# Performance work log

Hardware: AMD Instinct MI355X
Metric: run time of the kernel (lower is better)

Reference implementation:

```python
import jax, jax.numpy as jnp
import numpy as np

B, T, D = 256, 500, 3   # batch, time steps, input features (time, mag, err)
U, C = 512, 10          # PhasedLSTM units, n_classes
R_ON = 0.05             # open ratio of the phased time gate
ALPHA = 1e-3            # leak rate during closed phase
LN_EPS = 1e-3           # keras LayerNormalization default epsilon


def _glorot(key, shape):
    lim = np.sqrt(6.0 / (shape[0] + shape[1])).astype(np.float32)
    return jax.random.uniform(key, shape, jnp.float32, -lim, lim)


def setup_inputs() -> dict:
    key = jax.random.key(0)
    ks = jax.random.split(key, 12)
    x = jax.random.normal(ks[0], (B, T, D), jnp.float32)
    # monotonically increasing observation times per sample
    times = jnp.cumsum(jax.random.uniform(ks[1], (B, T), jnp.float32), axis=1)
    # layer 0 PhasedLSTM params (gate order i, f, g, o)
    W0 = _glorot(ks[2], (D, 4 * U)); R0 = _glorot(ks[3], (U, 4 * U)); b0 = jnp.zeros((4 * U,), jnp.float32)
    tau0 = jnp.exp(jax.random.uniform(ks[4], (U,), jnp.float32, 0.0, 3.0))
    s0 = jax.random.uniform(ks[5], (U,), jnp.float32) * tau0
    # layer 1
    W1 = _glorot(ks[6], (U, 4 * U)); R1 = _glorot(ks[7], (U, 4 * U)); b1 = jnp.zeros((4 * U,), jnp.float32)
    tau1 = jnp.exp(jax.random.uniform(ks[8], (U,), jnp.float32, 0.0, 3.0))
    s1 = jax.random.uniform(ks[9], (U,), jnp.float32) * tau1
    # per-layer LayerNorm params
    g0 = jnp.ones((U,), jnp.float32); be0 = jnp.zeros((U,), jnp.float32)
    g1 = jnp.ones((U,), jnp.float32); be1 = jnp.zeros((U,), jnp.float32)
    # classifier head
    Wf = _glorot(ks[10], (U, C)); bf = jnp.zeros((C,), jnp.float32)
    return dict(x=x, times=times, W0=W0, R0=R0, b0=b0, tau0=tau0, s0=s0, g0=g0, be0=be0,
                W1=W1, R1=R1, b1=b1, tau1=tau1, s1=s1, g1=g1, be1=be1, Wf=Wf, bf=bf)


def _layernorm(h, g, b):
    m = jnp.mean(h, axis=-1, keepdims=True)
    v = jnp.var(h, axis=-1, keepdims=True)
    return (h - m) * jax.lax.rsqrt(v + LN_EPS) * g + b


def _time_gate(t, tau, s):
    # t: [B], tau/s: [U] -> k: [B, U]
    phi = jnp.mod(t[:, None] - s, tau) / tau
    return jnp.where(phi < 0.5 * R_ON, 2.0 * phi / R_ON,
                     jnp.where(phi < R_ON, 2.0 - 2.0 * phi / R_ON, ALPHA * phi))


def _plstm_step(xi, ti, h, c, W, R, b, tau, s):
    z = xi @ W + h @ R + b                       # [B, 4U]
    i, f, g, o = jnp.split(z, 4, axis=-1)
    i = jax.nn.sigmoid(i); f = jax.nn.sigmoid(f); o = jax.nn.sigmoid(o)
    c_new = f * c + i * jnp.tanh(g)
    h_new = o * jnp.tanh(c_new)
    k = _time_gate(ti, tau, s)                   # phased time gate
    return k * h_new + (1.0 - k) * h, k * c_new + (1.0 - k) * c


def reference(x, times, W0, R0, b0, tau0, s0, g0, be0,
              W1, R1, b1, tau1, s1, g1, be1, Wf, bf):
    xt = jnp.transpose(x, (1, 0, 2))  # [T, B, D]
    tt = times.T                      # [T, B]
    zeros = jnp.zeros((x.shape[0], U), x.dtype)
    init = (zeros, zeros, zeros, zeros)

    def step(carry, inp):
        h0, c0, h1, c1 = carry
        xi, ti = inp
        h0n, c0n = _plstm_step(xi, ti, h0, c0, W0, R0, b0, tau0, s0)
        a0 = _layernorm(h0n, g0, be0)   # normed output feeds next layer; raw state is carried
        h1n, c1n = _plstm_step(a0, ti, h1, c1, W1, R1, b1, tau1, s1)
        a1 = _layernorm(h1n, g1, be1)
        probs = jax.nn.softmax(a1 @ Wf + bf)  # dropout is identity at inference
        return (h0n, c0n, h1n, c1n), probs

    _, out = jax.lax.scan(step, init, (xt, tt))  # out: [T, B, C]
    return jnp.transpose(out, (1, 0, 2))
```

## Files before the change

### kernel.cpp

```cpp
#include <hip/hip_runtime.h>
#include <hip/hip_bf16.h>


#define NB 256
#define NTHR 384
#define T_STEPS 500
#define RON 0.05f
#define ALPHA_LEAK 1e-3f

typedef short short8 __attribute__((ext_vector_type(8)));
typedef float f32x4 __attribute__((ext_vector_type(4)));
typedef unsigned long long ull;

#define OFF_WSWZ 0u
#define OFF_U1   6291456u
#define OFF_V1   6299648u
#define OFF_WFP  6307840u
#define OFF_UFV  6328320u
#define OFF_H0B  6328448u
#define OFF_H1B  6852736u
#define OFF_ST0  7377024u
#define OFF_ST1  7508096u
#define OFF_FLG0 7639168u
#define OFF_FLG1 7640192u
#define ZERO_BYTES 1312768u

#define SMEM_BYTES 156160

#define AT_LD(p)    __hip_atomic_load((p), __ATOMIC_RELAXED, __HIP_MEMORY_SCOPE_AGENT)
#define AT_ST(p, v) __hip_atomic_store((p), (v), __ATOMIC_RELAXED, __HIP_MEMORY_SCOPE_AGENT)

#define G2L(gp, lp) \
  __builtin_amdgcn_global_load_lds( \
      (const __attribute__((address_space(1))) void*)(gp), \
      (__attribute__((address_space(3))) void*)(lp), 16, 0, 16)

__device__ __forceinline__ short f2bf(float x) {
  unsigned u = __float_as_uint(x);
  unsigned r = (u + 0x7fffu + ((u >> 16) & 1u)) >> 16;
  return (short)r;
}
__device__ __forceinline__ float bf2f(short s) {
  return __uint_as_float(((unsigned)(unsigned short)s) << 16);
}
__device__ __forceinline__ float sigm(float x) { return 1.f / (1.f + __expf(-x)); }
__device__ __forceinline__ float tanh_f(float x) {
  float cx = fminf(fmaxf(x, -15.f), 15.f);
  float e = __expf(2.f * cx);
  return (e - 1.f) / (e + 1.f);
}
__device__ __forceinline__ float timegate(float t, float tau, float s) {
  float phi = fmodf(t - s, tau);
  if (phi < 0.f) phi += tau;
  phi /= tau;
  return phi < 0.5f * RON ? (2.f / RON) * phi
       : (phi < RON ? 2.f - (2.f / RON) * phi : ALPHA_LEAK * phi);
}
__device__ __forceinline__ int fragidx(int m, int k) {
  return ((((k >> 5) * 2 + (m >> 4)) * 64) + (((k >> 3) & 3) * 16) + (m & 15)) * 8 + (k & 7);
}

__global__ void prep_weights(const float* __restrict__ R0, const float* __restrict__ W1,
                             const float* __restrict__ R1, const float* __restrict__ g0,
                             short* __restrict__ Wswz) {
  int t = blockIdx.x * 256 + threadIdx.x;
  int lane = t & 63; int rest = t >> 6;
  int nf = rest & 1;  rest >>= 1;
  int kb = rest & 15; rest >>= 4;
  int ch = rest & 1;  rest >>= 1;
  int mm = rest % 3;  int slice = rest / 3;
  int c = ch * 32 + nf * 16 + (lane & 15);
  int gate = c >> 4;
  int unit = slice * 16 + (c & 15);
  int gcol = gate * 512 + unit;
  int k0 = kb * 32 + (lane >> 4) * 8;
  const float* src = (mm == 0) ? R0 : (mm == 1 ? W1 : R1);
  short8 o;
  #pragma unroll
  for (int e = 0; e < 8; ++e) {
    float v = src[(size_t)(k0 + e) * 2048 + gcol];
    if (mm == 1) v *= g0[k0 + e];
    o[e] = f2bf(v);
  }
  *(short8*)(Wswz + (size_t)t * 8) = o;
}

__global__ void prep_vecs(const float* __restrict__ W1, const float* __restrict__ g0,
                          const float* __restrict__ be0,
                          float* __restrict__ u1, float* __restrict__ v1) {
  int c = blockIdx.x * 256 + threadIdx.x;
  float su = 0.f, sv = 0.f;
  for (int k = 0; k < 512; ++k) {
    float w = W1[(size_t)k * 2048 + c];
    su += be0[k] * w; sv += g0[k] * w;
  }
  u1[c] = su; v1[c] = sv;
}

__global__ void prep_head(const float* __restrict__ Wf, const float* __restrict__ g1,
                          const float* __restrict__ be1, const float* __restrict__ bfv,
                          float* __restrict__ Wfp, float* __restrict__ ufv) {
  int t = blockIdx.x * 256 + threadIdx.x;
  if (t < 5120) {
    int kk = t / 640, rem = t - kk * 640, c = rem >> 6, l = rem & 63;
    int k = 8 * l + kk;
    Wfp[t] = g1[k] * Wf[k * 10 + c];
  }
  if (t < 10) {
    float su = bfv[t], sv = 0.f;
    for (int k = 0; k < 512; ++k) {
      float w = Wf[k * 10 + t];
      su += be1[k] * w; sv += g1[k] * w;
    }
    ufv[t] = su; ufv[16 + t] = sv;
  }
}

struct Ptrs {
  const float *x, *times, *W0, *b0, *tau0, *s0, *b1, *tau1, *s1;
  const float *u1v, *v1v, *Wfp, *ufv;
  short *H0b, *H1b;
  float *St0, *St1;
  unsigned *flag0, *flag1;
  float *out;
};

__launch_bounds__(NTHR, 1)
__global__ void plstm_persist(Ptrs P, const short* __restrict__ Wswz) {
  extern __shared__ char smem[];
  short* h0b  = (short*)smem;
  short* h1bL = (short*)(smem + 32768);
  float* h0f  = (float*)(smem + 98304);
  float* c0f = h0f + 512;
  float* h1f = h0f + 1024;
  float* c1f = h0f + 1536;
  float* mu0 = (float*)(smem + 106496); float* rs0 = mu0 + 32;
  float* mu1 = mu0 + 64;                float* rs1 = mu0 + 96;
  float* zbv = (float*)(smem + 107008);
  float* prm = (float*)(smem + 132736);
  float* wfl = (float*)(smem + 134784);
  float* ufl = (float*)(smem + 155264);
  float* xtb = (float*)(smem + 155392);
  float* xtb1 = (float*)(smem + 155904);

  const int tid = threadIdx.x;
  const int g = blockIdx.x & 7;
  const int slice = blockIdx.x >> 3;
  const int wid = tid >> 6, lane = tid & 63;
  const int mm = wid >> 1, ch = wid & 1;
  const int gm0 = g * 32;

  for (int i = tid; i < 2048; i += NTHR) h0f[i] = 0.f;
  for (int i = tid; i < 512; i += NTHR) {
    float v;
    if (i < 192)      { int f = i >> 6, c = i & 63; v = P.W0[f * 2048 + ((c >> 4) << 9) + slice * 16 + (c & 15)]; }
    else if (i < 256) { int c = i & 63; v = P.b0[((c >> 4) << 9) + slice * 16 + (c & 15)]; }
    else if (i < 320) { int c = i & 63; int gc = ((c >> 4) << 9) + slice * 16 + (c & 15);
                        v = P.b1[gc] + P.u1v[gc]; }
    else if (i < 384) { int c = i & 63; v = P.v1v[((c >> 4) << 9) + slice * 16 + (c & 15)]; }
    else if (i < 448) v = 0.f;
    else if (i < 464) v = P.tau0[slice * 16 + (i & 15)];
    else if (i < 480) v = P.s0[slice * 16 + (i & 15)];
    else if (i < 496) v = P.tau1[slice * 16 + (i & 15)];
    else              v = P.s1[slice * 16 + (i & 15)];
    prm[i] = v;
  }
  for (int i = tid; i < 5120; i += NTHR) wfl[i] = P.Wfp[i];
  if (tid < 32) ufl[tid] = P.ufv[tid];

  short8 wr[16][2];
  {
    const short* wb = Wswz + ((((size_t)slice * 3 + mm) * 2 + ch) * 32 * 64) * 8;
    #pragma unroll
    for (int kb = 0; kb < 16; ++kb)
      #pragma unroll
      for (int nf = 0; nf < 2; ++nf) {
        wr[kb][nf] = *(const short8*)(wb + ((kb * 2 + nf) * 64 + lane) * 8);
        asm volatile("" : "+v"(wr[kb][nf]));
      }
  }
  __syncthreads();

  for (int r = 0; r < T_STEPS + 2; ++r) {
    const int bufA = (r + 1) & 1;
    const int bufB = r & 1;
    short* h1s = h1bL + bufB * 16384;

    if (wid == 0) {
      const unsigned tgt = (unsigned)r;
      const unsigned* fp = P.flag0 + g * 32 + (lane & 31);
      for (int it_ = 0; it_ < 100000; ++it_) {
        unsigned v = (lane < 32) ? AT_LD(fp) : 0xFFFFFFFFu;
        if (__all((int)(v >= tgt))) break;
        __builtin_amdgcn_s_sleep(1);
      }
    } else if (wid == 4) {
      int m = lane & 31;
      if (lane < 32) {
        int step = (r < T_STEPS) ? r : (T_STEPS - 1);
        const float* xp = P.x + ((size_t)(gm0 + m) * T_STEPS + step) * 3;
        xtb[m * 4 + 0] = xp[0];
        xtb[m * 4 + 1] = xp[1];
        xtb[m * 4 + 2] = xp[2];
        xtb[m * 4 + 3] = P.times[(size_t)(gm0 + m) * T_STEPS + step];
      } else {
        int s1_ = (r >= 1) ? (r - 1) : 0;
        xtb1[m] = P.times[(size_t)(gm0 + m) * T_STEPS + s1_];
      }
    }
    __syncthreads();

    if (tid < 256) {
      const char* gA = (const char*)(P.H0b + ((size_t)bufA * 8 + g) * 16384);
      const char* gB = (const char*)(P.H1b + ((size_t)bufB * 8 + g) * 16384);
      char* lA = (char*)h0b;
      char* lB = (char*)h1s;
      #pragma unroll
      for (int k = 0; k < 8; ++k) {
        size_t off = (size_t)(k * 256 + tid) * 16;
        G2L(gA + off, lA + off);
        G2L(gB + off, lB + off);
      }
    } else if (wid == 5) {
      const int layer = lane >> 5, m = lane & 31;
      const float* base = layer ? (P.St1 + ((size_t)bufB * 8 + g) * 2048 + m * 64)
                                : (P.St0 + ((size_t)bufA * 8 + g) * 2048 + m * 64);
      const ull* bu = (const ull*)base;
      float s_ = 0.f, q_ = 0.f;
      #pragma unroll
      for (int sl = 0; sl < 32; ++sl) {
        ull v = AT_LD(bu + sl);
        s_ += __uint_as_float((unsigned)v);
        q_ += __uint_as_float((unsigned)(v >> 32));
      }
      float mu = s_ * (1.f / 512.f);
      float var = q_ * (1.f / 512.f) - mu * mu;
      float rs = rsqrtf(var + 1e-3f);
      if (layer == 0) { mu0[m] = mu; rs0[m] = rs; }
      else            { mu1[m] = mu; rs1[m] = rs; }
    }
    __syncthreads();
    float m1r = 0.f, r1r = 0.f;
    if (wid == 1) { m1r = mu1[slice]; r1r = rs1[slice]; }

    {
      f32x4 acc[2][2] = {};
      const short* asrc = (mm == 2) ? h1s : h0b;
      #pragma unroll
      for (int kb = 0; kb < 16; ++kb) {
        short8 a0 = *(const short8*)(asrc + ((kb * 2 + 0) * 64 + lane) * 8);
        short8 a1 = *(const short8*)(asrc + ((kb * 2 + 1) * 64 + lane) * 8);
        #pragma unroll
        for (int nf = 0; nf < 2; ++nf) {
          acc[0][nf] = __builtin_amdgcn_mfma_f32_16x16x32_bf16(a0, wr[kb][nf], acc[0][nf], 0, 0, 0);
          acc[1][nf] = __builtin_amdgcn_mfma_f32_16x16x32_bf16(a1, wr[kb][nf], acc[1][nf], 0, 0, 0);
        }
      }
      float* z = zbv + mm * 2144;
      #pragma unroll
      for (int mf = 0; mf < 2; ++mf)
        #pragma unroll
        for (int nf = 0; nf < 2; ++nf)
          #pragma unroll
          for (int q = 0; q < 4; ++q) {
            int row = mf * 16 + (lane >> 4) * 4 + q;
            int col = ch * 32 + nf * 16 + (lane & 15);
            z[row * 67 + col] = acc[mf][nf][q];
          }
    }
    __syncthreads();

    const bool l0act = (r < T_STEPS);
    const bool l1act = (r >= 1 && r <= T_STEPS);
    if (tid < 256 && l0act) {
      int m = tid >> 3, u0 = (tid & 7) << 1;
      float x0 = xtb[m * 4 + 0], x1 = xtb[m * 4 + 1], x2 = xtb[m * 4 + 2];
      float tmv = xtb[m * 4 + 3];
      unsigned pack = 0;
      float hnv[2];
      #pragma unroll
      for (int uu = 0; uu < 2; ++uu) {
        int u = u0 + uu, id = m * 16 + u;
        float zg4[4];
        #pragma unroll
        for (int q = 0; q < 4; ++q) {
          int c = q * 16 + u;
          zg4[q] = zbv[m * 67 + c] + prm[192 + c]
                 + x0 * prm[c] + x1 * prm[64 + c] + x2 * prm[128 + c];
        }
        float iv = sigm(zg4[0]), fv = sigm(zg4[1]), gv = tanh_f(zg4[2]), ov = sigm(zg4[3]);
        float cold = c0f[id], hold = h0f[id];
        float cp = fv * cold + iv * gv;
        float hp = ov * tanh_f(cp);
        float k = timegate(tmv, prm[448 + u], prm[464 + u]);
        float hn = k * hp + (1.f - k) * hold;
        float cn = k * cp + (1.f - k) * cold;
        h0f[id] = hn; c0f[id] = cn; hnv[uu] = hn;
        pack |= ((unsigned)(unsigned short)f2bf(hn)) << (16 * uu);
      }
      AT_ST((unsigned*)(P.H0b + ((size_t)bufB * 8 + g) * 16384 + fragidx(m, slice * 16 + u0)), pack);
      float sr = hnv[0] + hnv[1], qr = hnv[0] * hnv[0] + hnv[1] * hnv[1];
      sr += __shfl_down(sr, 4, 8); qr += __shfl_down(qr, 4, 8);
      sr += __shfl_down(sr, 2, 8); qr += __shfl_down(qr, 2, 8);
      sr += __shfl_down(sr, 1, 8); qr += __shfl_down(qr, 1, 8);
      if ((tid & 7) == 0) {
        ull pv = ((ull)__float_as_uint(qr) << 32) | __float_as_uint(sr);
        AT_ST((ull*)(P.St0 + ((size_t)bufB * 8 + g) * 2048) + m * 32 + slice, pv);
      }
    }
    #pragma unroll
    for (int pass = 0; pass < 2; ++pass) {
      int idx = -1;
      if (pass == 0 && tid >= 256) idx = tid - 256;
      if (pass == 1 && tid < 128)  idx = 128 + tid;
      if (idx >= 0 && l1act) {
        int m = idx >> 3, u0 = (idx & 7) << 1;
        float mu0m = mu0[m], rs0m = rs0[m];
        float tmv = xtb1[m];
        unsigned pack = 0;
        float hnv[2];
        #pragma unroll
        for (int uu = 0; uu < 2; ++uu) {
          int u = u0 + uu, id = m * 16 + u;
          float zg4[4];
          #pragma unroll
          for (int q = 0; q < 4; ++q) {
            int c = q * 16 + u;
            float zA = zbv[2144 + m * 67 + c];
            float zB = zbv[4288 + m * 67 + c];
            zg4[q] = rs0m * zA + zB + prm[256 + c] - mu0m * rs0m * prm[320 + c];
          }
          float iv = sigm(zg4[0]), fv = sigm(zg4[1]), gv = tanh_f(zg4[2]), ov = sigm(zg4[3]);
          float cold = c1f[id], hold = h1f[id];
          float cp = fv * cold + iv * gv;
          float hp = ov * tanh_f(cp);
          float k = timegate(tmv, prm[480 + u], prm[496 + u]);
          float hn = k * hp + (1.f - k) * hold;
          float cn = k * cp + (1.f - k) * cold;
          h1f[id] = hn; c1f[id] = cn; hnv[uu] = hn;
          pack |= ((unsigned)(unsigned short)f2bf(hn)) << (16 * uu);
        }
        AT_ST((unsigned*)(P.H1b + ((size_t)bufA * 8 + g) * 16384 + fragidx(m, slice * 16 + u0)), pack);
        float sr = hnv[0] + hnv[1], qr = hnv[0] * hnv[0] + hnv[1] * hnv[1];
        sr += __shfl_down(sr, 4, 8); qr += __shfl_down(qr, 4, 8);
        sr += __shfl_down(sr, 2, 8); qr += __shfl_down(qr, 2, 8);
        sr += __shfl_down(sr, 1, 8); qr += __shfl_down(qr, 1, 8);
        if ((idx & 7) == 0) {
          ull pv = ((ull)__float_as_uint(qr) << 32) | __float_as_uint(sr);
          AT_ST((ull*)(P.St1 + ((size_t)bufA * 8 + g) * 2048) + m * 32 + slice, pv);
        }
      }
    }
    __syncthreads();

    if (tid == 0 && r <= T_STEPS) {
      AT_ST(P.flag0 + g * 32 + slice, (unsigned)(r + 1));
    }
    if (wid == 1 && r >= 2) {
      int msam = slice;
      short8 hv8 = *(const short8*)(h1s + fragidx(msam, lane * 8));
      float lg[10];
      #pragma unroll
      for (int c = 0; c < 10; ++c) lg[c] = 0.f;
      #pragma unroll
      for (int kk = 0; kk < 8; ++kk) {
        float hv = bf2f(hv8[kk]);
        const float* wf = wfl + kk * 640 + lane;
        #pragma unroll
        for (int c = 0; c < 10; ++c) lg[c] += hv * wf[c * 64];
      }
      #pragma unroll
      for (int off = 32; off > 0; off >>= 1)
        #pragma unroll
        for (int c = 0; c < 10; ++c) lg[c] += __shfl_down(lg[c], off, 64);
      if (lane == 0) {
        float logit[10], mx = -1e30f;
        #pragma unroll
        for (int c = 0; c < 10; ++c) {
          logit[c] = r1r * lg[c] + ufl[c] - m1r * r1r * ufl[16 + c];
          mx = fmaxf(mx, logit[c]);
        }
        float ssum = 0.f;
        #pragma unroll
        for (int c = 0; c < 10; ++c) { logit[c] = expf(logit[c] - mx); ssum += logit[c]; }
        float inv = 1.f / ssum;
        float* op = P.out + ((size_t)(gm0 + msam) * T_STEPS + (r - 2)) * 10;
        #pragma unroll
        for (int c = 0; c < 10; ++c) op[c] = logit[c] * inv;
      }
    }
  }
}

extern "C" void kernel_launch(void* const* d_in, const int* in_sizes, int n_in,
                              void* d_out, int out_size, void* d_ws, size_t ws_size,
                              hipStream_t stream) {
  const float* x    = (const float*)d_in[0];
  const float* tms  = (const float*)d_in[1];
  const float* W0   = (const float*)d_in[2];
  const float* R0   = (const float*)d_in[3];
  const float* b0   = (const float*)d_in[4];
  const float* tau0 = (const float*)d_in[5];
  const float* s0   = (const float*)d_in[6];
  const float* g0   = (const float*)d_in[7];
  const float* be0  = (const float*)d_in[8];
  const float* W1   = (const float*)d_in[9];
  const float* R1   = (const float*)d_in[10];
  const float* b1   = (const float*)d_in[11];
  const float* tau1 = (const float*)d_in[12];
  const float* s1   = (const float*)d_in[13];
  const float* g1   = (const float*)d_in[14];
  const float* be1  = (const float*)d_in[15];
  const float* Wf   = (const float*)d_in[16];
  const float* bfv  = (const float*)d_in[17];

  char* ws = (char*)d_ws;
  short* Wswz = (short*)(ws + OFF_WSWZ);
  float* u1m  = (float*)(ws + OFF_U1);
  float* v1m  = (float*)(ws + OFF_V1);
  float* Wfpm = (float*)(ws + OFF_WFP);
  float* ufvm = (float*)(ws + OFF_UFV);

  Ptrs P;
  P.x = x; P.times = tms; P.W0 = W0; P.b0 = b0; P.tau0 = tau0; P.s0 = s0;
  P.b1 = b1; P.tau1 = tau1; P.s1 = s1;
  P.u1v = u1m; P.v1v = v1m; P.Wfp = Wfpm; P.ufv = ufvm;
  P.H0b = (short*)(ws + OFF_H0B);
  P.H1b = (short*)(ws + OFF_H1B);
  P.St0 = (float*)(ws + OFF_ST0);
  P.St1 = (float*)(ws + OFF_ST1);
  P.flag0 = (unsigned*)(ws + OFF_FLG0);
  P.flag1 = (unsigned*)(ws + OFF_FLG1);
  P.out = (float*)d_out;

  hipFuncSetAttribute(reinterpret_cast<const void*>(plstm_persist),
                      hipFuncAttributeMaxDynamicSharedMemorySize, SMEM_BYTES);

  prep_weights<<<1536, 256, 0, stream>>>(R0, W1, R1, g0, Wswz);
  prep_vecs<<<8, 256, 0, stream>>>(W1, g0, be0, u1m, v1m);
  prep_head<<<20, 256, 0, stream>>>(Wf, g1, be1, bfv, Wfpm, ufvm);
  hipMemsetAsync(ws + OFF_H0B, 0, ZERO_BYTES, stream);
  plstm_persist<<<NB, NTHR, SMEM_BYTES, stream>>>(P, Wswz);
}
```

Baseline: 5.245 ms.

## Warp-specialize persistent PLSTM kernel with LDS token sync and register-resident state

Adds two warps: one is a producer that waits on the cross-block flags and issues the global-to-LDS loads of h0/h1, and one handles LayerNorm statistics, next-step inputs, the flag publish and the softmax head. The six compute warps run the MFMAs and gate math. Workgroup-wide __syncthreads are replaced by LDS atomic token counters with spin-waits, and the h/c state moves from LDS into per-thread registers. The aim is to overlap the inter-block wait and load latency with compute and to cut barrier cost on the serial recurrence. In exchange it adds spin-wait overhead, a more fragile ordering protocol and higher register pressure.

```diff
diff --git a/kernel.cpp b/kernel.cpp
--- a/kernel.cpp
+++ b/kernel.cpp
@@ -3,7 +3,7 @@
 
 
 #define NB 256
-#define NTHR 384
+#define NTHR 512
 #define T_STEPS 500
 #define RON 0.05f
 #define ALPHA_LEAK 1e-3f
@@ -25,10 +25,13 @@
 #define OFF_FLG1 7640192u
 #define ZERO_BYTES 1312768u
 
-#define SMEM_BYTES 156160
+#define SMEM_BYTES 149504
 
 #define AT_LD(p)    __hip_atomic_load((p), __ATOMIC_RELAXED, __HIP_MEMORY_SCOPE_AGENT)
 #define AT_ST(p, v) __hip_atomic_store((p), (v), __ATOMIC_RELAXED, __HIP_MEMORY_SCOPE_AGENT)
+#define LDS_ADD(p)  __hip_atomic_fetch_add((p), 1u, __ATOMIC_RELEASE, __HIP_MEMORY_SCOPE_WORKGROUP)
+#define LDS_LD(p)   __hip_atomic_load((p), __ATOMIC_ACQUIRE, __HIP_MEMORY_SCOPE_WORKGROUP)
+#define LDS_ST(p,v) __hip_atomic_store((p), (v), __ATOMIC_RELEASE, __HIP_MEMORY_SCOPE_WORKGROUP)
 
 #define G2L(gp, lp) \
   __builtin_amdgcn_global_load_lds( \
@@ -130,18 +133,13 @@
   extern __shared__ char smem[];
   short* h0b  = (short*)smem;
   short* h1bL = (short*)(smem + 32768);
-  float* h0f  = (float*)(smem + 98304);
-  float* c0f = h0f + 512;
-  float* h1f = h0f + 1024;
-  float* c1f = h0f + 1536;
-  float* mu0 = (float*)(smem + 106496); float* rs0 = mu0 + 32;
-  float* mu1 = mu0 + 64;                float* rs1 = mu0 + 96;
-  float* zbv = (float*)(smem + 107008);
-  float* prm = (float*)(smem + 132736);
-  float* wfl = (float*)(smem + 134784);
-  float* ufl = (float*)(smem + 155264);
-  float* xtb = (float*)(smem + 155392);
-  float* xtb1 = (float*)(smem + 155904);
+  float* zbv  = (float*)(smem + 98304);
+  float* musL = (float*)(smem + 124032);
+  float* xtbL = (float*)(smem + 125056);
+  float* prm  = (float*)(smem + 126336);
+  float* wfl  = (float*)(smem + 128384);
+  float* ufl  = (float*)(smem + 148864);
+  unsigned* tok = (unsigned*)(smem + 148992);
 
   const int tid = threadIdx.x;
   const int g = blockIdx.x & 7;
@@ -150,7 +148,7 @@
   const int mm = wid >> 1, ch = wid & 1;
   const int gm0 = g * 32;
 
-  for (int i = tid; i < 2048; i += NTHR) h0f[i] = 0.f;
+  if (tid < 8) tok[tid] = 0u;
   for (int i = tid; i < 512; i += NTHR) {
     float v;
     if (i < 192)      { int f = i >> 6, c = i & 63; v = P.W0[f * 2048 + ((c >> 4) << 9) + slice * 16 + (c & 15)]; }
@@ -169,7 +167,7 @@
   if (tid < 32) ufl[tid] = P.ufv[tid];
 
   short8 wr[16][2];
-  {
+  if (wid < 6) {
     const short* wb = Wswz + ((((size_t)slice * 3 + mm) * 2 + ch) * 32 * 64) * 8;
     #pragma unroll
     for (int kb = 0; kb < 16; ++kb)
@@ -179,214 +177,270 @@
         asm volatile("" : "+v"(wr[kb][nf]));
       }
   }
+  float h0A0 = 0.f, h0A1 = 0.f, c0A0 = 0.f, c0A1 = 0.f;
+  float h1B0 = 0.f, h1B1 = 0.f, c1B0 = 0.f, c1B1 = 0.f;
+  float h1C0 = 0.f, h1C1 = 0.f, c1C0 = 0.f, c1C1 = 0.f;
   __syncthreads();
 
-  for (int r = 0; r < T_STEPS + 2; ++r) {
-    const int bufA = (r + 1) & 1;
-    const int bufB = r & 1;
-    short* h1s = h1bL + bufB * 16384;
-
-    if (wid == 0) {
-      const unsigned tgt = (unsigned)r;
-      const unsigned* fp = P.flag0 + g * 32 + (lane & 31);
-      for (int it_ = 0; it_ < 100000; ++it_) {
-        unsigned v = (lane < 32) ? AT_LD(fp) : 0xFFFFFFFFu;
-        if (__all((int)(v >= tgt))) break;
-        __builtin_amdgcn_s_sleep(1);
-      }
-    } else if (wid == 4) {
-      int m = lane & 31;
+  if (wid == 6) {
+    const char* gA = (const char*)(P.H0b + ((size_t)1 * 8 + g) * 16384);
+    const char* gB = (const char*)(P.H1b + ((size_t)0 * 8 + g) * 16384);
+    char* lA = (char*)h0b;
+    char* lB = (char*)h1bL;
+    #pragma unroll
+    for (int j = 0; j < 32; ++j) {
+      unsigned off = j * 1024u + (unsigned)lane * 16u;
+      G2L(gA + off, lA + off);
+      G2L(gB + off, lB + off);
+    }
+    asm volatile("s_waitcnt vmcnt(0)" ::: "memory");
+    if (lane == 0) { LDS_ST(&tok[2], 1u); LDS_ST(&tok[3], 1u); }
+  } else if (wid == 7) {
+    for (int it_ = 0; it_ < 200000; ++it_) { if (LDS_LD(&tok[2]) >= 1u) break; __builtin_amdgcn_s_sleep(1); }
+    {
+      const int layer = lane >> 5, m = lane & 31;
+      float* mus = musL;
+      mus[layer * 64 + m] = 0.f;
+      mus[layer * 64 + 32 + m] = rsqrtf(1e-3f);
+      float* xt = xtbL;
       if (lane < 32) {
-        int step = (r < T_STEPS) ? r : (T_STEPS - 1);
-        const float* xp = P.x + ((size_t)(gm0 + m) * T_STEPS + step) * 3;
-        xtb[m * 4 + 0] = xp[0];
-        xtb[m * 4 + 1] = xp[1];
-        xtb[m * 4 + 2] = xp[2];
-        xtb[m * 4 + 3] = P.times[(size_t)(gm0 + m) * T_STEPS + step];
+        const float* xp = P.x + ((size_t)(gm0 + lane) * T_STEPS) * 3;
+        xt[lane * 4 + 0] = xp[0]; xt[lane * 4 + 1] = xp[1]; xt[lane * 4 + 2] = xp[2];
+        xt[lane * 4 + 3] = P.times[(size_t)(gm0 + lane) * T_STEPS];
       } else {
-        int s1_ = (r >= 1) ? (r - 1) : 0;
-        xtb1[m] = P.times[(size_t)(gm0 + m) * T_STEPS + s1_];
+        int m2 = lane - 32;
+        xt[128 + m2] = P.times[(size_t)(gm0 + m2) * T_STEPS];
       }
     }
-    __syncthreads();
-
-    if (tid < 256) {
-      const char* gA = (const char*)(P.H0b + ((size_t)bufA * 8 + g) * 16384);
-      const char* gB = (const char*)(P.H1b + ((size_t)bufB * 8 + g) * 16384);
-      char* lA = (char*)h0b;
-      char* lB = (char*)h1s;
-      #pragma unroll
-      for (int k = 0; k < 8; ++k) {
-        size_t off = (size_t)(k * 256 + tid) * 16;
-        G2L(gA + off, lA + off);
-        G2L(gB + off, lB + off);
-      }
-    } else if (wid == 5) {
-      const int layer = lane >> 5, m = lane & 31;
-      const float* base = layer ? (P.St1 + ((size_t)bufB * 8 + g) * 2048 + m * 64)
-                                : (P.St0 + ((size_t)bufA * 8 + g) * 2048 + m * 64);
-      const ull* bu = (const ull*)base;
-      float s_ = 0.f, q_ = 0.f;
-      #pragma unroll
-      for (int sl = 0; sl < 32; ++sl) {
-        ull v = AT_LD(bu + sl);
-        s_ += __uint_as_float((unsigned)v);
-        q_ += __uint_as_float((unsigned)(v >> 32));
-      }
-      float mu = s_ * (1.f / 512.f);
-      float var = q_ * (1.f / 512.f) - mu * mu;
-      float rs = rsqrtf(var + 1e-3f);
-      if (layer == 0) { mu0[m] = mu; rs0[m] = rs; }
-      else            { mu1[m] = mu; rs1[m] = rs; }
-    }
-    __syncthreads();
-    float m1r = 0.f, r1r = 0.f;
-    if (wid == 1) { m1r = mu1[slice]; r1r = rs1[slice]; }
-
-    {
-      f32x4 acc[2][2] = {};
-      const short* asrc = (mm == 2) ? h1s : h0b;
-      #pragma unroll
-      for (int kb = 0; kb < 16; ++kb) {
-        short8 a0 = *(const short8*)(asrc + ((kb * 2 + 0) * 64 + lane) * 8);
-        short8 a1 = *(const short8*)(asrc + ((kb * 2 + 1) * 64 + lane) * 8);
-        #pragma unroll
-        for (int nf = 0; nf < 2; ++nf) {
-          acc[0][nf] = __builtin_amdgcn_mfma_f32_16x16x32_bf16(a0, wr[kb][nf], acc[0][nf], 0, 0, 0);
-          acc[1][nf] = __builtin_amdgcn_mfma_f32_16x16x32_bf16(a1, wr[kb][nf], acc[1][nf], 0, 0, 0);
-        }
-      }
-      float* z = zbv + mm * 2144;
-      #pragma unroll
-      for (int mf = 0; mf < 2; ++mf)
-        #pragma unroll
-        for (int nf = 0; nf < 2; ++nf)
-          #pragma unroll
-          for (int q = 0; q < 4; ++q) {
-            int row = mf * 16 + (lane >> 4) * 4 + q;
-            int col = ch * 32 + nf * 16 + (lane & 15);
-            z[row * 67 + col] = acc[mf][nf][q];
+    if (lane == 0) LDS_ST(&tok[4], 1u);
+  }
+
+  for (int r = 0; r <= T_STEPS + 1; ++r) {
+    if (wid < 6) {
+      { const unsigned tgt = (unsigned)(r + 1);
+        for (int it_ = 0; it_ < 400000; ++it_) {
+          if (LDS_LD(&tok[3]) >= tgt && LDS_LD(&tok[4]) >= tgt) break;
+          __builtin_amdgcn_s_sleep(1);
+        } }
+      if (r <= T_STEPS) {
+        f32x4 acc[2][2] = {};
+        const short* asrc = (mm == 2) ? (h1bL + (r & 1) * 16384) : h0b;
+        #pragma unroll
+        for (int kb = 0; kb < 16; ++kb) {
+          short8 a0 = *(const short8*)(asrc + ((kb * 2 + 0) * 64 + lane) * 8);
+          short8 a1 = *(const short8*)(asrc + ((kb * 2 + 1) * 64 + lane) * 8);
+          #pragma unroll
+          for (int nf = 0; nf < 2; ++nf) {
+            acc[0][nf] = __builtin_amdgcn_mfma_f32_16x16x32_bf16(a0, wr[kb][nf], acc[0][nf], 0, 0, 0);
+            acc[1][nf] = __builtin_amdgcn_mfma_f32_16x16x32_bf16(a1, wr[kb][nf], acc[1][nf], 0, 0, 0);
           }
-    }
-    __syncthreads();
-
-    const bool l0act = (r < T_STEPS);
-    const bool l1act = (r >= 1 && r <= T_STEPS);
-    if (tid < 256 && l0act) {
-      int m = tid >> 3, u0 = (tid & 7) << 1;
-      float x0 = xtb[m * 4 + 0], x1 = xtb[m * 4 + 1], x2 = xtb[m * 4 + 2];
-      float tmv = xtb[m * 4 + 3];
-      unsigned pack = 0;
-      float hnv[2];
-      #pragma unroll
-      for (int uu = 0; uu < 2; ++uu) {
-        int u = u0 + uu, id = m * 16 + u;
-        float zg4[4];
-        #pragma unroll
-        for (int q = 0; q < 4; ++q) {
-          int c = q * 16 + u;
-          zg4[q] = zbv[m * 67 + c] + prm[192 + c]
-                 + x0 * prm[c] + x1 * prm[64 + c] + x2 * prm[128 + c];
-        }
-        float iv = sigm(zg4[0]), fv = sigm(zg4[1]), gv = tanh_f(zg4[2]), ov = sigm(zg4[3]);
-        float cold = c0f[id], hold = h0f[id];
-        float cp = fv * cold + iv * gv;
-        float hp = ov * tanh_f(cp);
-        float k = timegate(tmv, prm[448 + u], prm[464 + u]);
-        float hn = k * hp + (1.f - k) * hold;
-        float cn = k * cp + (1.f - k) * cold;
-        h0f[id] = hn; c0f[id] = cn; hnv[uu] = hn;
-        pack |= ((unsigned)(unsigned short)f2bf(hn)) << (16 * uu);
-      }
-      AT_ST((unsigned*)(P.H0b + ((size_t)bufB * 8 + g) * 16384 + fragidx(m, slice * 16 + u0)), pack);
-      float sr = hnv[0] + hnv[1], qr = hnv[0] * hnv[0] + hnv[1] * hnv[1];
-      sr += __shfl_down(sr, 4, 8); qr += __shfl_down(qr, 4, 8);
-      sr += __shfl_down(sr, 2, 8); qr += __shfl_down(qr, 2, 8);
-      sr += __shfl_down(sr, 1, 8); qr += __shfl_down(qr, 1, 8);
-      if ((tid & 7) == 0) {
-        ull pv = ((ull)__float_as_uint(qr) << 32) | __float_as_uint(sr);
-        AT_ST((ull*)(P.St0 + ((size_t)bufB * 8 + g) * 2048) + m * 32 + slice, pv);
-      }
-    }
-    #pragma unroll
-    for (int pass = 0; pass < 2; ++pass) {
-      int idx = -1;
-      if (pass == 0 && tid >= 256) idx = tid - 256;
-      if (pass == 1 && tid < 128)  idx = 128 + tid;
-      if (idx >= 0 && l1act) {
-        int m = idx >> 3, u0 = (idx & 7) << 1;
-        float mu0m = mu0[m], rs0m = rs0[m];
-        float tmv = xtb1[m];
-        unsigned pack = 0;
-        float hnv[2];
+        }
+        float* z = zbv + mm * 2144;
+        #pragma unroll
+        for (int mf = 0; mf < 2; ++mf)
+          #pragma unroll
+          for (int nf = 0; nf < 2; ++nf)
+            #pragma unroll
+            for (int q = 0; q < 4; ++q) {
+              int row = mf * 16 + (lane >> 4) * 4 + q;
+              int col = ch * 32 + nf * 16 + (lane & 15);
+              z[row * 67 + col] = acc[mf][nf][q];
+            }
+      }
+      if (lane == 0) LDS_ADD(&tok[0]);
+      { const unsigned tgt = 6u * (unsigned)(r + 1);
+        for (int it_ = 0; it_ < (1 << 22); ++it_) { if (LDS_LD(&tok[0]) >= tgt) break; } }
+      const bool l0act = (r < T_STEPS);
+      const bool l1act = (r >= 1 && r <= T_STEPS);
+      const float* xt = xtbL + (r & 1) * 160;
+      const float* mus = musL + (r & 1) * 128;
+      if (tid < 256 && l0act) {
+        int m = tid >> 3, u0 = (tid & 7) << 1;
+        float x0 = xt[m * 4], x1 = xt[m * 4 + 1], x2 = xt[m * 4 + 2], tmv = xt[m * 4 + 3];
+        unsigned pack = 0; float hnv[2];
         #pragma unroll
         for (int uu = 0; uu < 2; ++uu) {
-          int u = u0 + uu, id = m * 16 + u;
-          float zg4[4];
+          int u = u0 + uu;
+          float zg[4];
           #pragma unroll
           for (int q = 0; q < 4; ++q) {
             int c = q * 16 + u;
-            float zA = zbv[2144 + m * 67 + c];
-            float zB = zbv[4288 + m * 67 + c];
-            zg4[q] = rs0m * zA + zB + prm[256 + c] - mu0m * rs0m * prm[320 + c];
+            zg[q] = zbv[m * 67 + c] + prm[192 + c]
+                  + x0 * prm[c] + x1 * prm[64 + c] + x2 * prm[128 + c];
           }
-          float iv = sigm(zg4[0]), fv = sigm(zg4[1]), gv = tanh_f(zg4[2]), ov = sigm(zg4[3]);
-          float cold = c1f[id], hold = h1f[id];
+          float iv = sigm(zg[0]), fv = sigm(zg[1]), gv = tanh_f(zg[2]), ov = sigm(zg[3]);
+          float cold = uu ? c0A1 : c0A0, hold = uu ? h0A1 : h0A0;
           float cp = fv * cold + iv * gv;
           float hp = ov * tanh_f(cp);
-          float k = timegate(tmv, prm[480 + u], prm[496 + u]);
+          float k = timegate(tmv, prm[448 + u], prm[464 + u]);
           float hn = k * hp + (1.f - k) * hold;
           float cn = k * cp + (1.f - k) * cold;
-          h1f[id] = hn; c1f[id] = cn; hnv[uu] = hn;
+          if (uu) { h0A1 = hn; c0A1 = cn; } else { h0A0 = hn; c0A0 = cn; }
+          hnv[uu] = hn;
           pack |= ((unsigned)(unsigned short)f2bf(hn)) << (16 * uu);
         }
-        AT_ST((unsigned*)(P.H1b + ((size_t)bufA * 8 + g) * 16384 + fragidx(m, slice * 16 + u0)), pack);
+        AT_ST((unsigned*)(P.H0b + ((size_t)(r & 1) * 8 + g) * 16384 + fragidx(m, slice * 16 + u0)), pack);
         float sr = hnv[0] + hnv[1], qr = hnv[0] * hnv[0] + hnv[1] * hnv[1];
         sr += __shfl_down(sr, 4, 8); qr += __shfl_down(qr, 4, 8);
         sr += __shfl_down(sr, 2, 8); qr += __shfl_down(qr, 2, 8);
         sr += __shfl_down(sr, 1, 8); qr += __shfl_down(qr, 1, 8);
-        if ((idx & 7) == 0) {
+        if ((tid & 7) == 0) {
           ull pv = ((ull)__float_as_uint(qr) << 32) | __float_as_uint(sr);
-          AT_ST((ull*)(P.St1 + ((size_t)bufA * 8 + g) * 2048) + m * 32 + slice, pv);
-        }
-      }
-    }
-    __syncthreads();
-
-    if (tid == 0 && r <= T_STEPS) {
-      AT_ST(P.flag0 + g * 32 + slice, (unsigned)(r + 1));
-    }
-    if (wid == 1 && r >= 2) {
-      int msam = slice;
-      short8 hv8 = *(const short8*)(h1s + fragidx(msam, lane * 8));
-      float lg[10];
+          AT_ST((ull*)(P.St0 + ((size_t)(r & 1) * 8 + g) * 2048) + m * 32 + slice, pv);
+        }
+      }
       #pragma unroll
-      for (int c = 0; c < 10; ++c) lg[c] = 0.f;
-      #pragma unroll
-      for (int kk = 0; kk < 8; ++kk) {
-        float hv = bf2f(hv8[kk]);
-        const float* wf = wfl + kk * 640 + lane;
-        #pragma unroll
-        for (int c = 0; c < 10; ++c) lg[c] += hv * wf[c * 64];
-      }
-      #pragma unroll
-      for (int off = 32; off > 0; off >>= 1)
-        #pragma unroll
-        for (int c = 0; c < 10; ++c) lg[c] += __shfl_down(lg[c], off, 64);
-      if (lane == 0) {
-        float logit[10], mx = -1e30f;
-        #pragma unroll
-        for (int c = 0; c < 10; ++c) {
-          logit[c] = r1r * lg[c] + ufl[c] - m1r * r1r * ufl[16 + c];
-          mx = fmaxf(mx, logit[c]);
-        }
-        float ssum = 0.f;
-        #pragma unroll
-        for (int c = 0; c < 10; ++c) { logit[c] = expf(logit[c] - mx); ssum += logit[c]; }
-        float inv = 1.f / ssum;
-        float* op = P.out + ((size_t)(gm0 + msam) * T_STEPS + (r - 2)) * 10;
-        #pragma unroll
-        for (int c = 0; c < 10; ++c) op[c] = logit[c] * inv;
+      for (int pass = 0; pass < 2; ++pass) {
+        int idx = -1;
+        if (pass == 0 && tid >= 256) idx = tid - 256;
+        if (pass == 1 && tid < 128)  idx = 128 + tid;
+        if (idx >= 0 && l1act) {
+          int m = idx >> 3, u0 = (idx & 7) << 1;
+          float mu0m = mus[m], rs0m = mus[32 + m];
+          float tmv = xt[128 + m];
+          unsigned pack = 0; float hnv[2];
+          #pragma unroll
+          for (int uu = 0; uu < 2; ++uu) {
+            int u = u0 + uu;
+            float zg[4];
+            #pragma unroll
+            for (int q = 0; q < 4; ++q) {
+              int c = q * 16 + u;
+              float zA = zbv[2144 + m * 67 + c];
+              float zB = zbv[4288 + m * 67 + c];
+              zg[q] = rs0m * zA + zB + prm[256 + c] - mu0m * rs0m * prm[320 + c];
+            }
+            float iv = sigm(zg[0]), fv = sigm(zg[1]), gv = tanh_f(zg[2]), ov = sigm(zg[3]);
+            float cold, hold;
+            if (pass == 0) { cold = uu ? c1B1 : c1B0; hold = uu ? h1B1 : h1B0; }
+            else           { cold = uu ? c1C1 : c1C0; hold = uu ? h1C1 : h1C0; }
+            float cp = fv * cold + iv * gv;
+            float hp = ov * tanh_f(cp);
+            float k = timegate(tmv, prm[480 + u], prm[496 + u]);
+            float hn = k * hp + (1.f - k) * hold;
+            float cn = k * cp + (1.f - k) * cold;
+            if (pass == 0) { if (uu) { h1B1 = hn; c1B1 = cn; } else { h1B0 = hn; c1B0 = cn; } }
+            else           { if (uu) { h1C1 = hn; c1C1 = cn; } else { h1C0 = hn; c1C0 = cn; } }
+            hnv[uu] = hn;
+            pack |= ((unsigned)(unsigned short)f2bf(hn)) << (16 * uu);
+          }
+          AT_ST((unsigned*)(P.H1b + ((size_t)((r + 1) & 1) * 8 + g) * 16384 + fragidx(m, slice * 16 + u0)), pack);
+          float sr = hnv[0] + hnv[1], qr = hnv[0] * hnv[0] + hnv[1] * hnv[1];
+          sr += __shfl_down(sr, 4, 8); qr += __shfl_down(qr, 4, 8);
+          sr += __shfl_down(sr, 2, 8); qr += __shfl_down(qr, 2, 8);
+          sr += __shfl_down(sr, 1, 8); qr += __shfl_down(qr, 1, 8);
+          if ((idx & 7) == 0) {
+            ull pv = ((ull)__float_as_uint(qr) << 32) | __float_as_uint(sr);
+            AT_ST((ull*)(P.St1 + ((size_t)((r + 1) & 1) * 8 + g) * 2048) + m * 32 + slice, pv);
+          }
+        }
+      }
+      asm volatile("s_waitcnt vmcnt(0)" ::: "memory");
+      if (lane == 0) LDS_ADD(&tok[1]);
+    } else if (wid == 6) {
+      const int rr = r + 1;
+      if (rr <= T_STEPS + 1) {
+        const unsigned tgt = (unsigned)rr;
+        const unsigned* fp = P.flag0 + g * 32 + (lane & 31);
+        for (int it_ = 0; it_ < 400000; ++it_) {
+          unsigned v = (lane < 32) ? AT_LD(fp) : 0xFFFFFFFFu;
+          if (__all((int)(v >= tgt))) break;
+          __builtin_amdgcn_s_sleep(1);
+        }
+        if (lane == 0) LDS_ST(&tok[2], (unsigned)(rr + 1));
+        const char* gA = (const char*)(P.H0b + ((size_t)((rr + 1) & 1) * 8 + g) * 16384);
+        const char* gB = (const char*)(P.H1b + ((size_t)(rr & 1) * 8 + g) * 16384);
+        char* lA = (char*)h0b;
+        char* lB = (char*)(h1bL + (rr & 1) * 16384);
+        #pragma unroll
+        for (int j = 0; j < 32; ++j) {
+          unsigned off = j * 1024u + (unsigned)lane * 16u;
+          G2L(gA + off, lA + off);
+          G2L(gB + off, lB + off);
+        }
+        asm volatile("s_waitcnt vmcnt(0)" ::: "memory");
+        if (lane == 0) LDS_ST(&tok[3], (unsigned)(rr + 1));
+      }
+    } else {
+      { const unsigned tgt = 6u * (unsigned)(r + 1);
+        for (int it_ = 0; it_ < 400000; ++it_) {
+          if (LDS_LD(&tok[1]) >= tgt) break;
+          __builtin_amdgcn_s_sleep(1);
+        } }
+      if (lane == 0) AT_ST(P.flag0 + g * 32 + slice, (unsigned)(r + 1));
+      const int rr = r + 1;
+      if (rr <= T_STEPS + 1) {
+        { const unsigned tgt = (unsigned)(rr + 1);
+          for (int it_ = 0; it_ < 400000; ++it_) {
+            if (LDS_LD(&tok[2]) >= tgt) break;
+            __builtin_amdgcn_s_sleep(1);
+          } }
+        const int layer = lane >> 5, m = lane & 31;
+        const float* base = layer
+            ? (P.St1 + ((size_t)(rr & 1) * 8 + g) * 2048 + m * 64)
+            : (P.St0 + ((size_t)((rr + 1) & 1) * 8 + g) * 2048 + m * 64);
+        const ull* bu = (const ull*)base;
+        float s_ = 0.f, q_ = 0.f;
+        #pragma unroll
+        for (int sl = 0; sl < 32; ++sl) {
+          ull v = AT_LD(bu + sl);
+          s_ += __uint_as_float((unsigned)v);
+          q_ += __uint_as_float((unsigned)(v >> 32));
+        }
+        float mu = s_ * (1.f / 512.f);
+        float var = q_ * (1.f / 512.f) - mu * mu;
+        float* mus = musL + (rr & 1) * 128;
+        mus[layer * 64 + m] = mu;
+        mus[layer * 64 + 32 + m] = rsqrtf(var + 1e-3f);
+        float* xt = xtbL + (rr & 1) * 160;
+        if (lane < 32) {
+          int step = (rr < T_STEPS) ? rr : (T_STEPS - 1);
+          const float* xp = P.x + ((size_t)(gm0 + lane) * T_STEPS + step) * 3;
+          xt[lane * 4 + 0] = xp[0]; xt[lane * 4 + 1] = xp[1]; xt[lane * 4 + 2] = xp[2];
+          xt[lane * 4 + 3] = P.times[(size_t)(gm0 + lane) * T_STEPS + step];
+        } else {
+          int m2 = lane - 32;
+          int s1_ = (rr >= 1) ? rr - 1 : 0;
+          if (s1_ > T_STEPS - 1) s1_ = T_STEPS - 1;
+          xt[128 + m2] = P.times[(size_t)(gm0 + m2) * T_STEPS + s1_];
+        }
+        if (lane == 0) LDS_ST(&tok[4], (unsigned)(rr + 1));
+      }
+      if (r >= 2) {
+        const int msam = slice;
+        const short* h1r = h1bL + (r & 1) * 16384;
+        short8 hv8 = *(const short8*)(h1r + fragidx(msam, lane * 8));
+        float lg[10];
+        #pragma unroll
+        for (int c = 0; c < 10; ++c) lg[c] = 0.f;
+        #pragma unroll
+        for (int kk = 0; kk < 8; ++kk) {
+          float hv = bf2f(hv8[kk]);
+          const float* wf = wfl + kk * 640 + lane;
+          #pragma unroll
+          for (int c = 0; c < 10; ++c) lg[c] += hv * wf[c * 64];
+        }
+        #pragma unroll
+        for (int off = 32; off > 0; off >>= 1)
+          #pragma unroll
+          for (int c = 0; c < 10; ++c) lg[c] += __shfl_down(lg[c], off, 64);
+        if (lane == 0) {
+          const float* mus = musL + (r & 1) * 128;
+          float m1 = mus[64 + msam], r1 = mus[96 + msam];
+          float logit[10], mx = -1e30f;
+          #pragma unroll
+          for (int c = 0; c < 10; ++c) {
+            logit[c] = r1 * lg[c] + ufl[c] - m1 * r1 * ufl[16 + c];
+            mx = fmaxf(mx, logit[c]);
+          }
+          float ssum = 0.f;
+          #pragma unroll
+          for (int c = 0; c < 10; ++c) { logit[c] = expf(logit[c] - mx); ssum += logit[c]; }
+          float inv = 1.f / ssum;
+          float* op = P.out + ((size_t)(gm0 + msam) * T_STEPS + (r - 2)) * 10;
+          #pragma unroll
+          for (int c = 0; c < 10; ++c) op[c] = logit[c] * inv;
+        }
       }
     }
   }
```

Result: slower. 7.193 ms (+37.1%).

## Widen block to 512 threads and keep recurrent state in registers

Applied to the files above, without the earlier changes.

The block grows from 384 to 512 threads. Two extra waves take over the flag polling/LN-stat gathering and the x/time prefetch plus classifier head, so the six MFMA waves do only the recurrent matmul. Layer-0 and layer-1 cell updates now run in a single pass over 512 threads instead of a layer-0 pass plus a two-pass layer-1 loop. Each thread keeps its h/c cell state in registers rather than shared memory. This cuts LDS traffic and serial element-wise passes, at the cost of more threads and register pressure, plus a duplicated spin-wait in two waves.

```diff
diff --git a/kernel.cpp b/kernel.cpp
--- a/kernel.cpp
+++ b/kernel.cpp
@@ -3,7 +3,7 @@
 
 
 #define NB 256
-#define NTHR 384
+#define NTHR 512
 #define T_STEPS 500
 #define RON 0.05f
 #define ALPHA_LEAK 1e-3f
@@ -25,7 +25,7 @@
 #define OFF_FLG1 7640192u
 #define ZERO_BYTES 1312768u
 
-#define SMEM_BYTES 156160
+#define SMEM_BYTES 147968
 
 #define AT_LD(p)    __hip_atomic_load((p), __ATOMIC_RELAXED, __HIP_MEMORY_SCOPE_AGENT)
 #define AT_ST(p, v) __hip_atomic_store((p), (v), __ATOMIC_RELAXED, __HIP_MEMORY_SCOPE_AGENT)
@@ -130,18 +130,12 @@
   extern __shared__ char smem[];
   short* h0b  = (short*)smem;
   short* h1bL = (short*)(smem + 32768);
-  float* h0f  = (float*)(smem + 98304);
-  float* c0f = h0f + 512;
-  float* h1f = h0f + 1024;
-  float* c1f = h0f + 1536;
-  float* mu0 = (float*)(smem + 106496); float* rs0 = mu0 + 32;
-  float* mu1 = mu0 + 64;                float* rs1 = mu0 + 96;
-  float* zbv = (float*)(smem + 107008);
-  float* prm = (float*)(smem + 132736);
-  float* wfl = (float*)(smem + 134784);
-  float* ufl = (float*)(smem + 155264);
-  float* xtb = (float*)(smem + 155392);
-  float* xtb1 = (float*)(smem + 155904);
+  float* zbv  = (float*)(smem + 98304);
+  float* mus  = (float*)(smem + 124032);
+  float* xtb  = (float*)(smem + 124544);
+  float* prm  = (float*)(smem + 125184);
+  float* wfl  = (float*)(smem + 127232);
+  float* ufl  = (float*)(smem + 147712);
 
   const int tid = threadIdx.x;
   const int g = blockIdx.x & 7;
@@ -150,7 +144,6 @@
   const int mm = wid >> 1, ch = wid & 1;
   const int gm0 = g * 32;
 
-  for (int i = tid; i < 2048; i += NTHR) h0f[i] = 0.f;
   for (int i = tid; i < 512; i += NTHR) {
     float v;
     if (i < 192)      { int f = i >> 6, c = i & 63; v = P.W0[f * 2048 + ((c >> 4) << 9) + slice * 16 + (c & 15)]; }
@@ -169,7 +162,7 @@
   if (tid < 32) ufl[tid] = P.ufv[tid];
 
   short8 wr[16][2];
-  {
+  if (wid < 6) {
     const short* wb = Wswz + ((((size_t)slice * 3 + mm) * 2 + ch) * 32 * 64) * 8;
     #pragma unroll
     for (int kb = 0; kb < 16; ++kb)
@@ -179,49 +172,40 @@
         asm volatile("" : "+v"(wr[kb][nf]));
       }
   }
+  float hS0 = 0.f, hS1 = 0.f, cS0 = 0.f, cS1 = 0.f;
   __syncthreads();
 
-  for (int r = 0; r < T_STEPS + 2; ++r) {
+  for (int r = 0; r <= T_STEPS + 1; ++r) {
     const int bufA = (r + 1) & 1;
     const int bufB = r & 1;
     short* h1s = h1bL + bufB * 16384;
 
     if (wid == 0) {
-      const unsigned tgt = (unsigned)r;
-      const unsigned* fp = P.flag0 + g * 32 + (lane & 31);
-      for (int it_ = 0; it_ < 100000; ++it_) {
-        unsigned v = (lane < 32) ? AT_LD(fp) : 0xFFFFFFFFu;
-        if (__all((int)(v >= tgt))) break;
-        __builtin_amdgcn_s_sleep(1);
-      }
-    } else if (wid == 4) {
-      int m = lane & 31;
-      if (lane < 32) {
-        int step = (r < T_STEPS) ? r : (T_STEPS - 1);
-        const float* xp = P.x + ((size_t)(gm0 + m) * T_STEPS + step) * 3;
-        xtb[m * 4 + 0] = xp[0];
-        xtb[m * 4 + 1] = xp[1];
-        xtb[m * 4 + 2] = xp[2];
-        xtb[m * 4 + 3] = P.times[(size_t)(gm0 + m) * T_STEPS + step];
-      } else {
-        int s1_ = (r >= 1) ? (r - 1) : 0;
-        xtb1[m] = P.times[(size_t)(gm0 + m) * T_STEPS + s1_];
-      }
-    }
-    __syncthreads();
-
-    if (tid < 256) {
+      { const unsigned tgt = (unsigned)r;
+        const unsigned* fp = P.flag0 + g * 32 + (lane & 31);
+        for (int it_ = 0; it_ < 200000; ++it_) {
+          unsigned v = (lane < 32) ? AT_LD(fp) : 0xFFFFFFFFu;
+          if (__all((int)(v >= tgt))) break;
+          __builtin_amdgcn_s_sleep(1);
+        } }
       const char* gA = (const char*)(P.H0b + ((size_t)bufA * 8 + g) * 16384);
       const char* gB = (const char*)(P.H1b + ((size_t)bufB * 8 + g) * 16384);
       char* lA = (char*)h0b;
       char* lB = (char*)h1s;
       #pragma unroll
-      for (int k = 0; k < 8; ++k) {
-        size_t off = (size_t)(k * 256 + tid) * 16;
+      for (int j = 0; j < 32; ++j) {
+        unsigned off = j * 1024u + (unsigned)lane * 16u;
         G2L(gA + off, lA + off);
         G2L(gB + off, lB + off);
       }
-    } else if (wid == 5) {
+    } else if (wid == 6) {
+      { const unsigned tgt = (unsigned)r;
+        const unsigned* fp = P.flag0 + g * 32 + (lane & 31);
+        for (int it_ = 0; it_ < 200000; ++it_) {
+          unsigned v = (lane < 32) ? AT_LD(fp) : 0xFFFFFFFFu;
+          if (__all((int)(v >= tgt))) break;
+          __builtin_amdgcn_s_sleep(1);
+        } }
       const int layer = lane >> 5, m = lane & 31;
       const float* base = layer ? (P.St1 + ((size_t)bufB * 8 + g) * 2048 + m * 64)
                                 : (P.St0 + ((size_t)bufA * 8 + g) * 2048 + m * 64);
@@ -235,15 +219,26 @@
       }
       float mu = s_ * (1.f / 512.f);
       float var = q_ * (1.f / 512.f) - mu * mu;
-      float rs = rsqrtf(var + 1e-3f);
-      if (layer == 0) { mu0[m] = mu; rs0[m] = rs; }
-      else            { mu1[m] = mu; rs1[m] = rs; }
+      mus[layer * 64 + m] = mu;
+      mus[layer * 64 + 32 + m] = rsqrtf(var + 1e-3f);
+    } else if (wid == 7) {
+      int m = lane & 31;
+      if (lane < 32) {
+        int step = (r < T_STEPS) ? r : (T_STEPS - 1);
+        const float* xp = P.x + ((size_t)(gm0 + m) * T_STEPS + step) * 3;
+        xtb[m * 4 + 0] = xp[0]; xtb[m * 4 + 1] = xp[1]; xtb[m * 4 + 2] = xp[2];
+        xtb[m * 4 + 3] = P.times[(size_t)(gm0 + m) * T_STEPS + step];
+      } else {
+        int s1_ = (r >= 1) ? r - 1 : 0;
+        if (s1_ > T_STEPS - 1) s1_ = T_STEPS - 1;
+        xtb[128 + m] = P.times[(size_t)(gm0 + m) * T_STEPS + s1_];
+      }
     }
     __syncthreads();
     float m1r = 0.f, r1r = 0.f;
-    if (wid == 1) { m1r = mu1[slice]; r1r = rs1[slice]; }
-
-    {
+    if (wid == 7) { m1r = mus[64 + slice]; r1r = mus[96 + slice]; }
+
+    if (wid < 6 && r <= T_STEPS) {
       f32x4 acc[2][2] = {};
       const short* asrc = (mm == 2) ? h1s : h0b;
       #pragma unroll
@@ -270,84 +265,75 @@
     }
     __syncthreads();
 
-    const bool l0act = (r < T_STEPS);
-    const bool l1act = (r >= 1 && r <= T_STEPS);
-    if (tid < 256 && l0act) {
-      int m = tid >> 3, u0 = (tid & 7) << 1;
-      float x0 = xtb[m * 4 + 0], x1 = xtb[m * 4 + 1], x2 = xtb[m * 4 + 2];
-      float tmv = xtb[m * 4 + 3];
-      unsigned pack = 0;
-      float hnv[2];
-      #pragma unroll
-      for (int uu = 0; uu < 2; ++uu) {
-        int u = u0 + uu, id = m * 16 + u;
-        float zg4[4];
-        #pragma unroll
-        for (int q = 0; q < 4; ++q) {
-          int c = q * 16 + u;
-          zg4[q] = zbv[m * 67 + c] + prm[192 + c]
-                 + x0 * prm[c] + x1 * prm[64 + c] + x2 * prm[128 + c];
+    {
+      const bool isL0 = (tid < 256);
+      const bool act = isL0 ? (r < T_STEPS) : (r >= 1 && r <= T_STEPS);
+      if (act) {
+        const int idx = isL0 ? tid : (tid - 256);
+        const int m = idx >> 3, u0 = (idx & 7) << 1;
+        unsigned pack = 0; float hnv[2];
+        if (isL0) {
+          float x0 = xtb[m * 4], x1 = xtb[m * 4 + 1], x2 = xtb[m * 4 + 2];
+          float tmv = xtb[m * 4 + 3];
+          #pragma unroll
+          for (int uu = 0; uu < 2; ++uu) {
+            int u = u0 + uu;
+            float zg[4];
+            #pragma unroll
+            for (int q = 0; q < 4; ++q) {
+              int c = q * 16 + u;
+              zg[q] = zbv[m * 67 + c] + prm[192 + c]
+                    + x0 * prm[c] + x1 * prm[64 + c] + x2 * prm[128 + c];
+            }
+            float iv = sigm(zg[0]), fv = sigm(zg[1]), gv = tanh_f(zg[2]), ov = sigm(zg[3]);
+            float cold = uu ? cS1 : cS0, hold = uu ? hS1 : hS0;
+            float cp = fv * cold + iv * gv;
+            float hp = ov * tanh_f(cp);
+            float k = timegate(tmv, prm[448 + u], prm[464 + u]);
+            float hn = k * hp + (1.f - k) * hold;
+            float cn = k * cp + (1.f - k) * cold;
+            if (uu) { hS1 = hn; cS1 = cn; } else { hS0 = hn; cS0 = cn; }
+            hnv[uu] = hn;
+            pack |= ((unsigned)(unsigned short)f2bf(hn)) << (16 * uu);
+          }
+          AT_ST((unsigned*)(P.H0b + ((size_t)bufB * 8 + g) * 16384 + fragidx(m, slice * 16 + u0)), pack);
+        } else {
+          float mu0m = mus[m], rs0m = mus[32 + m];
+          float tmv = xtb[128 + m];
+          #pragma unroll
+          for (int uu = 0; uu < 2; ++uu) {
+            int u = u0 + uu;
+            float zg[4];
+            #pragma unroll
+            for (int q = 0; q < 4; ++q) {
+              int c = q * 16 + u;
+              float zA = zbv[2144 + m * 67 + c];
+              float zB = zbv[4288 + m * 67 + c];
+              zg[q] = rs0m * zA + zB + prm[256 + c] - mu0m * rs0m * prm[320 + c];
+            }
+            float iv = sigm(zg[0]), fv = sigm(zg[1]), gv = tanh_f(zg[2]), ov = sigm(zg[3]);
+            float cold = uu ? cS1 : cS0, hold = uu ? hS1 : hS0;
+            float cp = fv * cold + iv * gv;
+            float hp = ov * tanh_f(cp);
+            float k = timegate(tmv, prm[480 + u], prm[496 + u]);
+            float hn = k * hp + (1.f - k) * hold;
+            float cn = k * cp + (1.f - k) * cold;
+            if (uu) { hS1 = hn; cS1 = cn; } else { hS0 = hn; cS0 = cn; }
+            hnv[uu] = hn;
+            pack |= ((unsigned)(unsigned short)f2bf(hn)) << (16 * uu);
+          }
+          AT_ST((unsigned*)(P.H1b + ((size_t)bufA * 8 + g) * 16384 + fragidx(m, slice * 16 + u0)), pack);
         }
-        float iv = sigm(zg4[0]), fv = sigm(zg4[1]), gv = tanh_f(zg4[2]), ov = sigm(zg4[3]);
-        float cold = c0f[id], hold = h0f[id];
-        float cp = fv * cold + iv * gv;
-        float hp = ov * tanh_f(cp);
-        float k = timegate(tmv, prm[448 + u], prm[464 + u]);
-        float hn = k * hp + (1.f - k) * hold;
-        float cn = k * cp + (1.f - k) * cold;
-        h0f[id] = hn; c0f[id] = cn; hnv[uu] = hn;
-        pack |= ((unsigned)(unsigned short)f2bf(hn)) << (16 * uu);
-      }
-      AT_ST((unsigned*)(P.H0b + ((size_t)bufB * 8 + g) * 16384 + fragidx(m, slice * 16 + u0)), pack);
-      float sr = hnv[0] + hnv[1], qr = hnv[0] * hnv[0] + hnv[1] * hnv[1];
-      sr += __shfl_down(sr, 4, 8); qr += __shfl_down(qr, 4, 8);
-      sr += __shfl_down(sr, 2, 8); qr += __shfl_down(qr, 2, 8);
-      sr += __shfl_down(sr, 1, 8); qr += __shfl_down(qr, 1, 8);
-      if ((tid & 7) == 0) {
-        ull pv = ((ull)__float_as_uint(qr) << 32) | __float_as_uint(sr);
-        AT_ST((ull*)(P.St0 + ((size_t)bufB * 8 + g) * 2048) + m * 32 + slice, pv);
-      }
-    }
-    #pragma unroll
-    for (int pass = 0; pass < 2; ++pass) {
-      int idx = -1;
-      if (pass == 0 && tid >= 256) idx = tid - 256;
-      if (pass == 1 && tid < 128)  idx = 128 + tid;
-      if (idx >= 0 && l1act) {
-        int m = idx >> 3, u0 = (idx & 7) << 1;
-        float mu0m = mu0[m], rs0m = rs0[m];
-        float tmv = xtb1[m];
-        unsigned pack = 0;
-        float hnv[2];
-        #pragma unroll
-        for (int uu = 0; uu < 2; ++uu) {
-          int u = u0 + uu, id = m * 16 + u;
-          float zg4[4];
-          #pragma unroll
-          for (int q = 0; q < 4; ++q) {
-            int c = q * 16 + u;
-            float zA = zbv[2144 + m * 67 + c];
-            float zB = zbv[4288 + m * 67 + c];
-            zg4[q] = rs0m * zA + zB + prm[256 + c] - mu0m * rs0m * prm[320 + c];
-          }
-          float iv = sigm(zg4[0]), fv = sigm(zg4[1]), gv = tanh_f(zg4[2]), ov = sigm(zg4[3]);
-          float cold = c1f[id], hold = h1f[id];
-          float cp = fv * cold + iv * gv;
-          float hp = ov * tanh_f(cp);
-          float k = timegate(tmv, prm[480 + u], prm[496 + u]);
-          float hn = k * hp + (1.f - k) * hold;
-          float cn = k * cp + (1.f - k) * cold;
-          h1f[id] = hn; c1f[id] = cn; hnv[uu] = hn;
-          pack |= ((unsigned)(unsigned short)f2bf(hn)) << (16 * uu);
-        }
-        AT_ST((unsigned*)(P.H1b + ((size_t)bufA * 8 + g) * 16384 + fragidx(m, slice * 16 + u0)), pack);
         float sr = hnv[0] + hnv[1], qr = hnv[0] * hnv[0] + hnv[1] * hnv[1];
         sr += __shfl_down(sr, 4, 8); qr += __shfl_down(qr, 4, 8);
         sr += __shfl_down(sr, 2, 8); qr += __shfl_down(qr, 2, 8);
         sr += __shfl_down(sr, 1, 8); qr += __shfl_down(qr, 1, 8);
         if ((idx & 7) == 0) {
           ull pv = ((ull)__float_as_uint(qr) << 32) | __float_as_uint(sr);
-          AT_ST((ull*)(P.St1 + ((size_t)bufA * 8 + g) * 2048) + m * 32 + slice, pv);
+          ull* sp = isL0
+              ? ((ull*)(P.St0 + ((size_t)bufB * 8 + g) * 2048) + m * 32 + slice)
+              : ((ull*)(P.St1 + ((size_t)bufA * 8 + g) * 2048) + m * 32 + slice);
+          AT_ST(sp, pv);
         }
       }
     }
@@ -356,8 +342,8 @@
     if (tid == 0 && r <= T_STEPS) {
       AT_ST(P.flag0 + g * 32 + slice, (unsigned)(r + 1));
     }
-    if (wid == 1 && r >= 2) {
-      int msam = slice;
+    if (wid == 7 && r >= 2) {
+      const int msam = slice;
       short8 hv8 = *(const short8*)(h1s + fragidx(msam, lane * 8));
       float lg[10];
       #pragma unroll
```

Measured after the change: 5.900 ms. 12.5% more time.
